# Optimization experiments

Measured on AMD Instinct MI355X. Metric: run time of the kernel, lower is better.

Reference implementation:

```python
import jax, jax.numpy as jnp
import numpy as np


def conv3x3(y, w, b):
    # y: [1, Cin, H, W], w: [Cout, Cin, 3, 3] -> [1, Cout, H, W], stride 1, pad 1
    out = jax.lax.conv_general_dilated(
        y, w, window_strides=(1, 1), padding='SAME',
        dimension_numbers=('NCHW', 'OIHW', 'NCHW'))
    return out + b[None, :, None, None]


def setup_inputs() -> dict:
    key = jax.random.key(0)
    ks = jax.random.split(key, 8)
    N, Cin, Cy, H, W, inter = 1024, 1024, 256, 128, 128, 256
    x = jax.random.normal(ks[0], (N, Cin), dtype=jnp.float32)
    y = jax.random.normal(ks[1], (1, Cy, H, W), dtype=jnp.float32)
    # weights initialized ~N(0, 0.01) as in the torch module; biases zero
    g_w = jax.random.normal(ks[2], (inter, Cy, 3, 3), dtype=jnp.float32) * 0.01
    g_b = jnp.zeros((inter,), dtype=jnp.float32)
    phi_w = jax.random.normal(ks[3], (inter, Cy, 3, 3), dtype=jnp.float32) * 0.01
    phi_b = jnp.zeros((inter,), dtype=jnp.float32)
    theta_w = jax.random.normal(ks[4], (inter, Cin), dtype=jnp.float32) * 0.01
    theta_b = jnp.zeros((inter,), dtype=jnp.float32)
    concat_w = jax.random.normal(ks[5], (1, 2 * inter, 1, 1), dtype=jnp.float32) * 0.01
    gamma = jnp.ones((1,), dtype=jnp.float32)  # torch inits 0; use 1 for nontrivial output
    return {"x": x, "y": y, "g_w": g_w, "g_b": g_b, "phi_w": phi_w,
            "phi_b": phi_b, "theta_w": theta_w, "theta_b": theta_b,
            "concat_w": concat_w, "gamma": gamma}


def reference(x, y, g_w, g_b, phi_w, phi_b, theta_w, theta_b, concat_w, gamma):
    inter = g_w.shape[0]
    H, W = y.shape[2], y.shape[3]
    g_y = conv3x3(y, g_w, g_b)          # [1, inter, H, W]
    phi_y = conv3x3(y, phi_w, phi_b)    # [1, inter, H, W]
    theta_x = x @ theta_w.T + theta_b   # [N, inter]
    # 1x1 conv over cat([theta repeated, phi repeated], dim=1) decomposes exactly
    # (linearity of the 1x1 conv, no bias) into two dot products + broadcast add,
    # avoiding the [N, 2*inter, H, W] materialization.
    w = concat_w[0, :, 0, 0]            # [2*inter]
    w_t, w_p = w[:inter], w[inter:]
    s_theta = theta_x @ w_t             # [N]
    s_phi = jnp.einsum('chw,c->hw', phi_y[0], w_p).reshape(-1)  # [H*W]
    f = jax.nn.softmax(s_theta[:, None] + s_phi[None, :], axis=1)  # [N, H*W]
    # g_y.squeeze() -> [inter,H,W]; permute(1,2,0).view(H*W, inter)
    g_flat = jnp.transpose(g_y[0], (1, 2, 0)).reshape(H * W, inter)
    z = gamma * (f @ g_flat)            # [N, inter]
    return z
```

## Files before the change

### kernel.cpp

```cpp
#include <hip/hip_runtime.h>

#define HWDIM 128
#define NPIX  (HWDIM * HWDIM)
#define CY    256
#define INTER 256
#define KTAPS 9
#define WEN   (CY * KTAPS)
#define NW1   32
#define NCS   8
#define CPG   32
#define NPART2 256
#define NRG   4


__device__ __forceinline__ float wave_red_sum(float v) {
    #pragma unroll
    for (int s = 32; s > 0; s >>= 1) v += __shfl_down(v, s, 64);
    return v;
}
__device__ __forceinline__ float wave_red_max(float v) {
    #pragma unroll
    for (int s = 32; s > 0; s >>= 1) v = fmaxf(v, __shfl_down(v, s, 64));
    return v;
}

__global__ void k1_wepart(const float* __restrict__ phi_w,
                          const float* __restrict__ concat_w,
                          float* __restrict__ we_part) {
    int b = blockIdx.x, t = threadIdx.x;
    int cg = b / 9, og = b - cg * 9;
    int o = og * 256 + t;
    const float* pw = phi_w + o;
    float acc = 0.f;
    #pragma unroll
    for (int j = 0; j < 8; ++j) {
        int c = cg * 8 + j;
        acc = fmaf(concat_w[INTER + c], pw[c * WEN], acc);
    }
    we_part[cg * WEN + o] = acc;
}

__global__ void k2a_taps(const float* __restrict__ y,
                         const float* __restrict__ we_part,
                         float* __restrict__ A) {
    __shared__ float swe[CPG * KTAPS];
    int t = threadIdx.x;
    int pg = blockIdx.x & 63;
    int cg = blockIdx.x >> 6;

    for (int i = t; i < CPG * KTAPS; i += 256) {
        float s = 0.f;
        #pragma unroll
        for (int p = 0; p < NW1; ++p)
            s += we_part[p * WEN + cg * CPG * KTAPS + i];
        swe[i] = s;
    }
    __syncthreads();

    int pix = pg * 256 + t;
    float acc[KTAPS];
    #pragma unroll
    for (int k = 0; k < KTAPS; ++k) acc[k] = 0.f;

    const float* yp = y + (size_t)cg * CPG * NPIX + pix;
    #pragma unroll 4
    for (int ch = 0; ch < CPG; ++ch) {
        float yv = yp[ch * NPIX];
        const float* wk = swe + ch * KTAPS;
        #pragma unroll
        for (int k = 0; k < KTAPS; ++k)
            acc[k] = fmaf(wk[k], yv, acc[k]);
    }
    #pragma unroll
    for (int k = 0; k < KTAPS; ++k)
        A[(size_t)(cg * KTAPS + k) * NPIX + pix] = acc[k];
}

__global__ void k2b_sphi(const float* __restrict__ A,
                         float* __restrict__ sphi,
                         float* __restrict__ partials) {
    __shared__ float sred[256];
    int t = threadIdx.x;
    int tg = t >> 6, pl = t & 63;
    int pix = blockIdx.x * 64 + pl;
    int h = pix >> 7, w = pix & 127;

    int idx[KTAPS]; bool val[KTAPS];
    #pragma unroll
    for (int kh = 0; kh < 3; ++kh)
        #pragma unroll
        for (int kw = 0; kw < 3; ++kw) {
            int hh = h + kh - 1, ww = w + kw - 1;
            int k = kh * 3 + kw;
            val[k] = ((unsigned)hh < HWDIM) & ((unsigned)ww < HWDIM);
            idx[k] = hh * HWDIM + ww;
        }

    float acc = 0.f;
    #pragma unroll
    for (int cc = 0; cc < 2; ++cc) {
        const float* Ab = A + (size_t)(tg * 2 + cc) * KTAPS * NPIX;
        #pragma unroll
        for (int k = 0; k < KTAPS; ++k)
            if (val[k]) acc += Ab[(size_t)k * NPIX + idx[k]];
    }
    sred[t] = acc;
    __syncthreads();

    if (t < 64) {
        float v = sred[t] + sred[t + 64] + sred[t + 128] + sred[t + 192];
        sphi[blockIdx.x * 64 + t] = v;
        float m = wave_red_max(v);
        float M = __shfl(m, 0, 64);
        float e = expf(v - M);
        float s = wave_red_sum(e);
        if (t == 0) {
            partials[2 * blockIdx.x]     = M;
            partials[2 * blockIdx.x + 1] = s;
        }
    }
}

__global__ void k4_q(const float* __restrict__ y,
                     const float* __restrict__ sphi,
                     const float* __restrict__ partials,
                     float* __restrict__ q_part) {
    __shared__ float sp[34 * 130];
    __shared__ float s4m[4], s4s[4];
    __shared__ float sq4[4][KTAPS];
    int cy = blockIdx.x & 255;
    int rg = blockIdx.x >> 8;
    int t = threadIdx.x;
    int wid = t >> 6, lane = t & 63;

    float m = partials[2 * t], s = partials[2 * t + 1];
    float wm = wave_red_max(m);
    if (lane == 0) s4m[wid] = wm;
    __syncthreads();
    float M = fmaxf(fmaxf(s4m[0], s4m[1]), fmaxf(s4m[2], s4m[3]));
    float sv = s * expf(m - M);
    float wsum = wave_red_sum(sv);
    if (lane == 0) s4s[wid] = wsum;
    __syncthreads();
    float invS = 1.f / (s4s[0] + s4s[1] + s4s[2] + s4s[3]);

    for (int i = t; i < 34 * 130; i += 256) {
        int r = i / 130, col = i - r * 130;
        int gr = rg * 32 + r - 1, gc = col - 1;
        float v = 0.f;
        if ((unsigned)gr < HWDIM && (unsigned)gc < HWDIM)
            v = expf(sphi[gr * HWDIM + gc] - M) * invS;
        sp[i] = v;
    }
    __syncthreads();

    const float* yc = y + (size_t)cy * NPIX;
    float acc[KTAPS];
    #pragma unroll
    for (int k = 0; k < KTAPS; ++k) acc[k] = 0.f;
    int c = t & 127, vg = t >> 7;

    for (int j = 0; j < 4; ++j) {
        int lr0 = vg * 4 + j * 8;
        float pv[6][3];
        #pragma unroll
        for (int u = 0; u < 6; ++u)
            #pragma unroll
            for (int v = 0; v < 3; ++v)
                pv[u][v] = sp[(lr0 + u) * 130 + c + v];
        #pragma unroll
        for (int dr = 0; dr < 4; ++dr) {
            float yv = yc[(rg * 32 + lr0 + dr) * HWDIM + c];
            #pragma unroll
            for (int kh = 0; kh < 3; ++kh)
                #pragma unroll
                for (int kw = 0; kw < 3; ++kw)
                    acc[kh * 3 + kw] = fmaf(pv[dr + 2 - kh][2 - kw], yv,
                                            acc[kh * 3 + kw]);
        }
    }

    #pragma unroll
    for (int k = 0; k < KTAPS; ++k) {
        float v = wave_red_sum(acc[k]);
        if (lane == 0) sq4[wid][k] = v;
    }
    __syncthreads();
    if (t < KTAPS)
        q_part[rg * WEN + cy * KTAPS + t] =
            sq4[0][t] + sq4[1][t] + sq4[2][t] + sq4[3][t];
}

__global__ void k5_row(const float* __restrict__ g_w,
                       const float* __restrict__ q_part,
                       float* __restrict__ row_part) {
    __shared__ float s4[4];
    int t = threadIdx.x;
    int c = blockIdx.x & 255, half = blockIdx.x >> 8;
    int base = half * (WEN / 2);

    const float* gw = g_w + (size_t)c * WEN;
    float acc = 0.f;
    #pragma unroll
    for (int j = 0; j < 5; ++j) {
        int o = base + j * 256 + t;
        if (o < base + WEN / 2) {
            float qv = q_part[o] + q_part[WEN + o] +
                       q_part[2 * WEN + o] + q_part[3 * WEN + o];
            acc = fmaf(gw[o], qv, acc);
        }
    }
    float v = wave_red_sum(acc);
    int wid = t >> 6, lane = t & 63;
    if (lane == 0) s4[wid] = v;
    __syncthreads();
    if (t == 0)
        row_part[half * 256 + c] = s4[0] + s4[1] + s4[2] + s4[3];
}

__global__ void k6_bcast(const float* __restrict__ row_part,
                         const float* __restrict__ g_b,
                         const float* __restrict__ gamma,
                         float* __restrict__ out, int out_size) {
    __shared__ float sr[256];
    int t = threadIdx.x;
    sr[t] = gamma[0] * (g_b[t] + row_part[t] + row_part[256 + t]);
    __syncthreads();
    int gid = blockIdx.x * 256 + t;
    if (gid < out_size) out[gid] = sr[t];
}

extern "C" void kernel_launch(void* const* d_in, const int* in_sizes, int n_in,
                              void* d_out, int out_size, void* d_ws, size_t ws_size,
                              hipStream_t stream) {
    const float* y        = (const float*)d_in[1];
    const float* g_w      = (const float*)d_in[2];
    const float* g_b      = (const float*)d_in[3];
    const float* phi_w    = (const float*)d_in[4];
    const float* concat_w = (const float*)d_in[8];
    const float* gamma    = (const float*)d_in[9];
    float* out = (float*)d_out;

    float* ws       = (float*)d_ws;
    float* we_part  = ws;
    float* A        = we_part + NW1 * WEN;
    float* sphi     = A + (size_t)NCS * KTAPS * NPIX;
    float* partials = sphi + NPIX;
    float* q_part   = partials + 2 * NPART2;
    float* row_part = q_part + NRG * WEN;
    (void)in_sizes; (void)n_in; (void)ws_size;

    hipLaunchKernelGGL(k1_wepart, dim3(288),      dim3(256), 0, stream,
                       phi_w, concat_w, we_part);
    hipLaunchKernelGGL(k2a_taps,  dim3(64 * NCS), dim3(256), 0, stream,
                       y, we_part, A);
    hipLaunchKernelGGL(k2b_sphi,  dim3(NPART2),   dim3(256), 0, stream,
                       A, sphi, partials);
    hipLaunchKernelGGL(k4_q,      dim3(NRG * CY), dim3(256), 0, stream,
                       y, sphi, partials, q_part);
    hipLaunchKernelGGL(k5_row,    dim3(512),      dim3(256), 0, stream,
                       g_w, q_part, row_part);
    hipLaunchKernelGGL(k6_bcast,  dim3((out_size + 255) / 256), dim3(256), 0,
                       stream, row_part, g_b, gamma, out, out_size);
}
```

Before: 117.1 us.

## Fuse phi-score, local softmax and q reduction; merge row and broadcast kernels

The pipeline goes from six kernels to four. The phi-score stencil is now computed inside the q kernel over a 2-row tile with halo, using a per-tile max and sum (online softmax) instead of a separate global-partials pass. The final kernel rescales the 64 per-tile q partials, does the g_w row dot product and writes the broadcast output in one place. This saves launches and round trips of sphi through memory. In exchange the A stencil is recomputed for halo rows, and the last kernel runs only 16 blocks, which may underuse the GPU.

```diff
diff --git a/kernel.cpp b/kernel.cpp
--- a/kernel.cpp
+++ b/kernel.cpp
@@ -9,8 +9,9 @@
 #define NW1   32
 #define NCS   8
 #define CPG   32
-#define NPART2 256
-#define NRG   4
+#define NRG   64
+#define RPG   2
+#define NCYG  8
 
 
 __device__ __forceinline__ float wave_red_sum(float v) {
@@ -24,9 +25,10 @@
     return v;
 }
 
-__global__ void k1_wepart(const float* __restrict__ phi_w,
-                          const float* __restrict__ concat_w,
-                          float* __restrict__ we_part) {
+__global__ __launch_bounds__(256)
+void k1_wepart(const float* __restrict__ phi_w,
+               const float* __restrict__ concat_w,
+               float* __restrict__ we_part) {
     int b = blockIdx.x, t = threadIdx.x;
     int cg = b / 9, og = b - cg * 9;
     int o = og * 256 + t;
@@ -40,13 +42,13 @@
     we_part[cg * WEN + o] = acc;
 }
 
-__global__ void k2a_taps(const float* __restrict__ y,
-                         const float* __restrict__ we_part,
-                         float* __restrict__ A) {
+__global__ __launch_bounds__(256)
+void k2_taps(const float* __restrict__ y,
+             const float* __restrict__ we_part,
+             float* __restrict__ A) {
     __shared__ float swe[CPG * KTAPS];
     int t = threadIdx.x;
-    int pg = blockIdx.x & 63;
-    int cg = blockIdx.x >> 6;
+    int pg = blockIdx.x & 63, cg = blockIdx.x >> 6;
 
     for (int i = t; i < CPG * KTAPS; i += 256) {
         float s = 0.f;
@@ -61,7 +63,6 @@
     float acc[KTAPS];
     #pragma unroll
     for (int k = 0; k < KTAPS; ++k) acc[k] = 0.f;
-
     const float* yp = y + (size_t)cg * CPG * NPIX + pix;
     #pragma unroll 4
     for (int ch = 0; ch < CPG; ++ch) {
@@ -76,158 +77,150 @@
         A[(size_t)(cg * KTAPS + k) * NPIX + pix] = acc[k];
 }
 
-__global__ void k2b_sphi(const float* __restrict__ A,
-                         float* __restrict__ sphi,
-                         float* __restrict__ partials) {
-    __shared__ float sred[256];
-    int t = threadIdx.x;
-    int tg = t >> 6, pl = t & 63;
-    int pix = blockIdx.x * 64 + pl;
-    int h = pix >> 7, w = pix & 127;
-
-    int idx[KTAPS]; bool val[KTAPS];
-    #pragma unroll
-    for (int kh = 0; kh < 3; ++kh)
-        #pragma unroll
-        for (int kw = 0; kw < 3; ++kw) {
-            int hh = h + kh - 1, ww = w + kw - 1;
-            int k = kh * 3 + kw;
-            val[k] = ((unsigned)hh < HWDIM) & ((unsigned)ww < HWDIM);
-            idx[k] = hh * HWDIM + ww;
-        }
-
-    float acc = 0.f;
-    #pragma unroll
-    for (int cc = 0; cc < 2; ++cc) {
-        const float* Ab = A + (size_t)(tg * 2 + cc) * KTAPS * NPIX;
-        #pragma unroll
-        for (int k = 0; k < KTAPS; ++k)
-            if (val[k]) acc += Ab[(size_t)k * NPIX + idx[k]];
-    }
-    sred[t] = acc;
-    __syncthreads();
-
-    if (t < 64) {
-        float v = sred[t] + sred[t + 64] + sred[t + 128] + sred[t + 192];
-        sphi[blockIdx.x * 64 + t] = v;
-        float m = wave_red_max(v);
-        float M = __shfl(m, 0, 64);
-        float e = expf(v - M);
-        float s = wave_red_sum(e);
-        if (t == 0) {
-            partials[2 * blockIdx.x]     = M;
-            partials[2 * blockIdx.x + 1] = s;
-        }
-    }
-}
-
-__global__ void k4_q(const float* __restrict__ y,
-                     const float* __restrict__ sphi,
-                     const float* __restrict__ partials,
-                     float* __restrict__ q_part) {
-    __shared__ float sp[34 * 130];
-    __shared__ float s4m[4], s4s[4];
-    __shared__ float sq4[4][KTAPS];
-    int cy = blockIdx.x & 255;
-    int rg = blockIdx.x >> 8;
+__global__ __launch_bounds__(256)
+void k3_q(const float* __restrict__ y,
+          const float* __restrict__ A,
+          float* __restrict__ q_part,
+          float* __restrict__ MS) {
+    __shared__ float ssph[4 * 130];
+    __shared__ float s4[4];
+    int b = blockIdx.x;
+    int rg = b >> 3, cyg = b & 7;
     int t = threadIdx.x;
     int wid = t >> 6, lane = t & 63;
-
-    float m = partials[2 * t], s = partials[2 * t + 1];
+    const int R0 = rg * RPG;
+
+    for (int i = t; i < 4 * 130; i += 256) {
+        int r = i / 130, col = i - r * 130;
+        int h = R0 + r - 1, w = col - 1;
+        float v;
+        if ((unsigned)h < (unsigned)HWDIM && (unsigned)w < (unsigned)HWDIM) {
+            v = 0.f;
+            #pragma unroll
+            for (int kh = 0; kh < 3; ++kh) {
+                int hh = h + kh - 1;
+                if ((unsigned)hh >= (unsigned)HWDIM) continue;
+                #pragma unroll
+                for (int kw = 0; kw < 3; ++kw) {
+                    int ww = w + kw - 1;
+                    if ((unsigned)ww >= (unsigned)HWDIM) continue;
+                    int k = kh * 3 + kw;
+                    int idx = hh * HWDIM + ww;
+                    #pragma unroll
+                    for (int cg = 0; cg < NCS; ++cg)
+                        v += A[(size_t)(cg * KTAPS + k) * NPIX + idx];
+                }
+            }
+        } else {
+            v = -INFINITY;
+        }
+        ssph[i] = v;
+    }
+    __syncthreads();
+
+    float m = -INFINITY;
+    for (int i = t; i < 4 * 130; i += 256) m = fmaxf(m, ssph[i]);
     float wm = wave_red_max(m);
-    if (lane == 0) s4m[wid] = wm;
-    __syncthreads();
-    float M = fmaxf(fmaxf(s4m[0], s4m[1]), fmaxf(s4m[2], s4m[3]));
-    float sv = s * expf(m - M);
-    float wsum = wave_red_sum(sv);
-    if (lane == 0) s4s[wid] = wsum;
-    __syncthreads();
-    float invS = 1.f / (s4s[0] + s4s[1] + s4s[2] + s4s[3]);
-
-    for (int i = t; i < 34 * 130; i += 256) {
-        int r = i / 130, col = i - r * 130;
-        int gr = rg * 32 + r - 1, gc = col - 1;
+    if (lane == 0) s4[wid] = wm;
+    __syncthreads();
+    float M = fmaxf(fmaxf(s4[0], s4[1]), fmaxf(s4[2], s4[3]));
+
+    for (int i = t; i < 4 * 130; i += 256) ssph[i] = expf(ssph[i] - M);
+    __syncthreads();
+
+    {
+        int r = 1 + (t >> 7), col = 1 + (t & 127);
+        float sv = ssph[r * 130 + col];
+        float ws = wave_red_sum(sv);
+        if (lane == 0) s4[wid] = ws;
+        __syncthreads();
+        if (cyg == 0 && t == 0) {
+            MS[rg * 2]     = M;
+            MS[rg * 2 + 1] = s4[0] + s4[1] + s4[2] + s4[3];
+        }
+    }
+
+    const int c2 = lane * 2;
+    float pv[4][4];
+    #pragma unroll
+    for (int r = 0; r < 4; ++r)
+        #pragma unroll
+        for (int j = 0; j < 4; ++j)
+            pv[r][j] = ssph[r * 130 + c2 + j];
+
+    const int base_cy = cyg * 32 + wid * 8;
+    for (int ch = 0; ch < 8; ++ch) {
+        const float* yc = y + (size_t)(base_cy + ch) * NPIX;
+        float2 y0 = ((const float2*)(yc + (size_t)R0 * HWDIM))[lane];
+        float2 y1 = ((const float2*)(yc + (size_t)(R0 + 1) * HWDIM))[lane];
+        float acc[KTAPS];
+        #pragma unroll
+        for (int kh = 0; kh < 3; ++kh)
+            #pragma unroll
+            for (int kw = 0; kw < 3; ++kw) {
+                int k = kh * 3 + kw;
+                acc[k] = pv[2 - kh][2 - kw] * y0.x + pv[2 - kh][3 - kw] * y0.y
+                       + pv[3 - kh][2 - kw] * y1.x + pv[3 - kh][3 - kw] * y1.y;
+            }
+        #pragma unroll
+        for (int k = 0; k < KTAPS; ++k) {
+            float v = wave_red_sum(acc[k]);
+            if (lane == 0)
+                q_part[(size_t)rg * WEN + (base_cy + ch) * KTAPS + k] = v;
+        }
+    }
+}
+
+__global__ __launch_bounds__(256)
+void k4_out(const float* __restrict__ g_w,
+            const float* __restrict__ g_b,
+            const float* __restrict__ gamma,
+            const float* __restrict__ q_part,
+            const float* __restrict__ MS,
+            float* __restrict__ out, int out_size) {
+    __shared__ float sms[2 * NRG];
+    __shared__ float sfac[NRG];
+    __shared__ float sq[WEN];
+    __shared__ float srow[16];
+    int t = threadIdx.x, b = blockIdx.x;
+
+    if (t < 2 * NRG) sms[t] = MS[t];
+    __syncthreads();
+
+    float M = -INFINITY;
+    #pragma unroll 8
+    for (int i = 0; i < NRG; ++i) M = fmaxf(M, sms[2 * i]);
+    float S = 0.f;
+    #pragma unroll 8
+    for (int i = 0; i < NRG; ++i) S += expf(sms[2 * i] - M) * sms[2 * i + 1];
+    if (t < NRG) sfac[t] = expf(sms[2 * t] - M) / S;
+    __syncthreads();
+
+    for (int o = t; o < WEN; o += 256) {
         float v = 0.f;
-        if ((unsigned)gr < HWDIM && (unsigned)gc < HWDIM)
-            v = expf(sphi[gr * HWDIM + gc] - M) * invS;
-        sp[i] = v;
-    }
-    __syncthreads();
-
-    const float* yc = y + (size_t)cy * NPIX;
-    float acc[KTAPS];
-    #pragma unroll
-    for (int k = 0; k < KTAPS; ++k) acc[k] = 0.f;
-    int c = t & 127, vg = t >> 7;
-
-    for (int j = 0; j < 4; ++j) {
-        int lr0 = vg * 4 + j * 8;
-        float pv[6][3];
-        #pragma unroll
-        for (int u = 0; u < 6; ++u)
-            #pragma unroll
-            for (int v = 0; v < 3; ++v)
-                pv[u][v] = sp[(lr0 + u) * 130 + c + v];
-        #pragma unroll
-        for (int dr = 0; dr < 4; ++dr) {
-            float yv = yc[(rg * 32 + lr0 + dr) * HWDIM + c];
-            #pragma unroll
-            for (int kh = 0; kh < 3; ++kh)
-                #pragma unroll
-                for (int kw = 0; kw < 3; ++kw)
-                    acc[kh * 3 + kw] = fmaf(pv[dr + 2 - kh][2 - kw], yv,
-                                            acc[kh * 3 + kw]);
-        }
-    }
-
-    #pragma unroll
-    for (int k = 0; k < KTAPS; ++k) {
-        float v = wave_red_sum(acc[k]);
-        if (lane == 0) sq4[wid][k] = v;
-    }
-    __syncthreads();
-    if (t < KTAPS)
-        q_part[rg * WEN + cy * KTAPS + t] =
-            sq4[0][t] + sq4[1][t] + sq4[2][t] + sq4[3][t];
-}
-
-__global__ void k5_row(const float* __restrict__ g_w,
-                       const float* __restrict__ q_part,
-                       float* __restrict__ row_part) {
-    __shared__ float s4[4];
-    int t = threadIdx.x;
-    int c = blockIdx.x & 255, half = blockIdx.x >> 8;
-    int base = half * (WEN / 2);
-
+        #pragma unroll 8
+        for (int rg = 0; rg < NRG; ++rg)
+            v = fmaf(sfac[rg], q_part[(size_t)rg * WEN + o], v);
+        sq[o] = v;
+    }
+    __syncthreads();
+
+    int cl = t >> 4, sub = t & 15;
+    int c = b * 16 + cl;
     const float* gw = g_w + (size_t)c * WEN;
     float acc = 0.f;
-    #pragma unroll
-    for (int j = 0; j < 5; ++j) {
-        int o = base + j * 256 + t;
-        if (o < base + WEN / 2) {
-            float qv = q_part[o] + q_part[WEN + o] +
-                       q_part[2 * WEN + o] + q_part[3 * WEN + o];
-            acc = fmaf(gw[o], qv, acc);
-        }
-    }
-    float v = wave_red_sum(acc);
-    int wid = t >> 6, lane = t & 63;
-    if (lane == 0) s4[wid] = v;
-    __syncthreads();
-    if (t == 0)
-        row_part[half * 256 + c] = s4[0] + s4[1] + s4[2] + s4[3];
-}
-
-__global__ void k6_bcast(const float* __restrict__ row_part,
-                         const float* __restrict__ g_b,
-                         const float* __restrict__ gamma,
-                         float* __restrict__ out, int out_size) {
-    __shared__ float sr[256];
-    int t = threadIdx.x;
-    sr[t] = gamma[0] * (g_b[t] + row_part[t] + row_part[256 + t]);
-    __syncthreads();
-    int gid = blockIdx.x * 256 + t;
-    if (gid < out_size) out[gid] = sr[t];
+    for (int j = sub; j < WEN; j += 16) acc = fmaf(gw[j], sq[j], acc);
+    #pragma unroll
+    for (int s = 8; s > 0; s >>= 1) acc += __shfl_down(acc, s, 16);
+    if (sub == 0) srow[cl] = gamma[0] * (g_b[c] + acc);
+    __syncthreads();
+
+    int c0 = b * 16;
+    for (int pass = 0; pass < 64; ++pass) {
+        int r = pass * 16 + cl;
+        int gid = r * 256 + c0 + sub;
+        if (gid < out_size) out[gid] = srow[sub];
+    }
 }
 
 extern "C" void kernel_launch(void* const* d_in, const int* in_sizes, int n_in,
@@ -244,22 +237,16 @@
     float* ws       = (float*)d_ws;
     float* we_part  = ws;
     float* A        = we_part + NW1 * WEN;
-    float* sphi     = A + (size_t)NCS * KTAPS * NPIX;
-    float* partials = sphi + NPIX;
-    float* q_part   = partials + 2 * NPART2;
-    float* row_part = q_part + NRG * WEN;
+    float* q_part   = A + (size_t)NCS * KTAPS * NPIX;
+    float* MS       = q_part + (size_t)NRG * WEN;
     (void)in_sizes; (void)n_in; (void)ws_size;
 
-    hipLaunchKernelGGL(k1_wepart, dim3(288),      dim3(256), 0, stream,
+    hipLaunchKernelGGL(k1_wepart, dim3(288), dim3(256), 0, stream,
                        phi_w, concat_w, we_part);
-    hipLaunchKernelGGL(k2a_taps,  dim3(64 * NCS), dim3(256), 0, stream,
+    hipLaunchKernelGGL(k2_taps,   dim3(512), dim3(256), 0, stream,
                        y, we_part, A);
-    hipLaunchKernelGGL(k2b_sphi,  dim3(NPART2),   dim3(256), 0, stream,
-                       A, sphi, partials);
-    hipLaunchKernelGGL(k4_q,      dim3(NRG * CY), dim3(256), 0, stream,
-                       y, sphi, partials, q_part);
-    hipLaunchKernelGGL(k5_row,    dim3(512),      dim3(256), 0, stream,
-                       g_w, q_part, row_part);
-    hipLaunchKernelGGL(k6_bcast,  dim3((out_size + 255) / 256), dim3(256), 0,
-                       stream, row_part, g_b, gamma, out, out_size);
-}
+    hipLaunchKernelGGL(k3_q,      dim3(512), dim3(256), 0, stream,
+                       y, A, q_part, MS);
+    hipLaunchKernelGGL(k4_out,    dim3(16),  dim3(256), 0, stream,
+                       g_w, g_b, gamma, q_part, MS, out, out_size);
+}
```

Result: slower. 191.8 us (+63.9%).
